# Performance work log

Measured on AMD Instinct MI355X. Metric: run time of the kernel, lower is better.

The kernel has to match this reference:

```python
import jax, jax.numpy as jnp
import numpy as np

BN_EPS = 1e-5


def _fps(xyz, n_centers):
    """Furthest point sampling. xyz: (B,N,3) -> idx (B,n_centers) int32.
    Deterministic start at index 0 (torch version uses randint start)."""
    B, N, _ = xyz.shape
    batch_ar = jnp.arange(B)

    def step(carry, _):
        distances, farthest = carry  # (B,N), (B,)
        center = xyz[batch_ar, farthest]  # (B,3)
        d = jnp.sum((xyz - center[:, None, :]) ** 2, axis=-1)  # (B,N)
        distances = jnp.minimum(distances, d)
        new_far = jnp.argmax(distances, axis=-1)
        return (distances, new_far), farthest

    init = (jnp.full((B, N), jnp.inf, dtype=xyz.dtype),
            jnp.zeros((B,), dtype=jnp.int32))
    _, idxs = jax.lax.scan(step, init, None, length=n_centers)  # (n_centers, B)
    return idxs.T  # (B, n_centers)


def _knn_group(xyz, centers, k):
    """xyz:(B,N,3), centers:(B,M,3) -> patches (B,M,k,3) center-relative."""
    # (B,M,N) squared distances
    dists = jnp.sum((centers[:, :, None, :] - xyz[:, None, :, :]) ** 2, axis=-1)
    _, idx = jax.lax.top_k(-dists, k)  # (B,M,k) smallest distances
    # gather neighbor coords: (B,M,k,3)
    patches = jnp.take_along_axis(xyz[:, None, :, :], idx[..., None], axis=2)
    return patches - centers[:, :, None, :]


def _bn_eval(x, gamma, beta):
    # BatchNorm1d in eval mode: running_mean=0, running_var=1
    return x * (gamma / jnp.sqrt(1.0 + BN_EPS)) + beta


def _mini_pointnet(patches, W1, b1, g1, bt1, W2, b2, g2, bt2, W3, b3, g3, bt3):
    B, M, k, C = patches.shape
    x = patches.reshape(B * M * k, C)
    x = jax.nn.relu(_bn_eval(x @ W1 + b1, g1, bt1))
    x = jax.nn.relu(_bn_eval(x @ W2 + b2, g2, bt2))
    x = jax.nn.relu(_bn_eval(x @ W3 + b3, g3, bt3))
    x = x.reshape(B * M, k, -1).max(axis=1)
    return x.reshape(B, M, -1)


def setup_inputs() -> dict:
    key = jax.random.key(0)
    ks = jax.random.split(key, 8)
    B, N = 16, 16384
    embed = 256

    def lin(kk, fan_in, fan_out):
        bound = 1.0 / np.sqrt(fan_in)
        k1, k2 = jax.random.split(kk)
        W = jax.random.uniform(k1, (fan_in, fan_out), jnp.float32, -bound, bound)
        b = jax.random.uniform(k2, (fan_out,), jnp.float32, -bound, bound)
        return W, b

    W1, b1 = lin(ks[1], 3, 64)
    W2, b2 = lin(ks[2], 64, 128)
    W3, b3 = lin(ks[3], 128, embed)
    return {
        "xyz": jax.random.normal(ks[0], (B, N, 3), jnp.float32),
        "W1": W1, "b1": b1, "g1": jnp.ones((64,)), "bt1": jnp.zeros((64,)),
        "W2": W2, "b2": b2, "g2": jnp.ones((128,)), "bt2": jnp.zeros((128,)),
        "W3": W3, "b3": b3, "g3": jnp.ones((embed,)), "bt3": jnp.zeros((embed,)),
        "n_centers": 256,
        "k": 32,
    }


def reference(xyz, W1, b1, g1, bt1, W2, b2, g2, bt2, W3, b3, g3, bt3,
              n_centers, k):
    center_idx = _fps(xyz, n_centers)  # (B, M)
    centers = jnp.take_along_axis(xyz, center_idx[..., None], axis=1)  # (B,M,3)
    patches = _knn_group(xyz, centers, k)  # (B,M,k,3)
    tokens = _mini_pointnet(patches, W1, b1, g1, bt1, W2, b2, g2, bt2,
                            W3, b3, g3, bt3)
    return tokens, centers
```

## Files before the change

kernel.cpp:

```cpp
#include <hip/hip_runtime.h>

constexpr int B   = 16;
constexpr int N   = 16384;
constexpr int M   = 256;
constexpr int K   = 32;
constexpr int EMB = 256;

__device__ __forceinline__ float sqdist(float px, float py, float pz,
                                        float cx, float cy, float cz) {
  float dx = __fsub_rn(px, cx);
  float dy = __fsub_rn(py, cy);
  float dz = __fsub_rn(pz, cz);
  return __fadd_rn(__fadd_rn(__fmul_rn(dx, dx), __fmul_rn(dy, dy)),
                   __fmul_rn(dz, dz));
}

constexpr int FT = 1024;
constexpr int FW = FT / 64;

#define FPS_REP16(X) X(0) X(1) X(2) X(3) X(4) X(5) X(6) X(7) X(8) X(9) \
  X(10) X(11) X(12) X(13) X(14) X(15)

__global__ __launch_bounds__(FT) void fps_kernel(
    const float* __restrict__ xyz, float* __restrict__ centers) {
  const int b = blockIdx.x;
  const int tid = threadIdx.x;
  const float* base = xyz + (size_t)b * N * 3;
  const float4* b4 = (const float4*)base;

#define FPS_DECL(i) float ds##i = __builtin_inff();
  FPS_REP16(FPS_DECL)
#undef FPS_DECL

  __shared__ float s_pv[2][FW];
  __shared__ int s_pn[2][FW];

  float cx = base[0], cy = base[1], cz = base[2];

  const int f0 = tid * 12;

  for (int it = 0; it < M; ++it) {
    if (tid == 0) {
      float* co = centers + ((size_t)b * M + it) * 3;
      co[0] = cx; co[1] = cy; co[2] = cz;
    }
    const int p = it & 1;

    float bv = -1.0f;
    int bj = 0;

#define FPS_UPD(dn, j, X, Y, Z) {                          \
    float dx = __fsub_rn((X), cx);                         \
    float dy = __fsub_rn((Y), cy);                         \
    float dz = __fsub_rn((Z), cz);                         \
    float dd = __fadd_rn(__fadd_rn(__fmul_rn(dx, dx),      \
                                   __fmul_rn(dy, dy)),     \
                         __fmul_rn(dz, dz));               \
    float nd = fminf(dn, dd);                              \
    dn = nd;                                               \
    bool g = nd > bv;                                      \
    bv = g ? nd : bv;                                      \
    bj = g ? (j) : bj; }

#define FPS_CHUNK(c, dA, dB, dC, dD) {                     \
    float4 qa = b4[f0 + (c) * 3 + 0];                      \
    float4 qb = b4[f0 + (c) * 3 + 1];                      \
    float4 qc = b4[f0 + (c) * 3 + 2];                      \
    FPS_UPD(dA, (c) * 4 + 0, qa.x, qa.y, qa.z)             \
    FPS_UPD(dB, (c) * 4 + 1, qa.w, qb.x, qb.y)             \
    FPS_UPD(dC, (c) * 4 + 2, qb.z, qb.w, qc.x)             \
    FPS_UPD(dD, (c) * 4 + 3, qc.y, qc.z, qc.w) }

    FPS_CHUNK(0, ds0, ds1, ds2, ds3)
    FPS_CHUNK(1, ds4, ds5, ds6, ds7)
    FPS_CHUNK(2, ds8, ds9, ds10, ds11)
    FPS_CHUNK(3, ds12, ds13, ds14, ds15)
#undef FPS_CHUNK
#undef FPS_UPD

    int bn = (tid << 4) + bj;

#pragma unroll
    for (int mm = 32; mm >= 1; mm >>= 1) {
      float ov = __shfl_xor(bv, mm, 64);
      int on = __shfl_xor(bn, mm, 64);
      if (ov > bv || (ov == bv && on < bn)) { bv = ov; bn = on; }
    }
    if ((tid & 63) == 0) { s_pv[p][tid >> 6] = bv; s_pn[p][tid >> 6] = bn; }
    __syncthreads();

    float v = s_pv[p][0];
    int n = s_pn[p][0];
#pragma unroll
    for (int w = 1; w < FW; ++w) {
      float ov = s_pv[p][w];
      int on = s_pn[p][w];
      if (ov > v || (ov == v && on < n)) { v = ov; n = on; }
    }
    cx = base[(size_t)n * 3 + 0];
    cy = base[(size_t)n * 3 + 1];
    cz = base[(size_t)n * 3 + 2];
  }
}

constexpr int KT = 256;
constexpr int CAP = 512;
constexpr int NBUCKET = 1024;

__global__ __launch_bounds__(KT) void knn_kernel(
    const float* __restrict__ xyz, const float* __restrict__ centers,
    float* __restrict__ patches) {
  const int blk = blockIdx.x;
  const int b = blk >> 8;
  const int tid = threadIdx.x;
  const float* base = xyz + (size_t)b * N * 3;

  __shared__ int hist[NBUCKET];
  __shared__ unsigned cb[CAP];
  __shared__ int ci[CAP];
  __shared__ int s_nin, s_ncand, s_tb;
  __shared__ int s_wsum[KT / 64];
  __shared__ float s_cc[3];

  if (tid == 0) {
    const float* c = centers + (size_t)blk * 3;
    s_cc[0] = c[0]; s_cc[1] = c[1]; s_cc[2] = c[2];
    s_nin = 0; s_ncand = 0;
  }
  for (int i = tid; i < NBUCKET; i += KT) hist[i] = 0;
  __syncthreads();

  const float cx = s_cc[0], cy = s_cc[1], cz = s_cc[2];

  for (int n = tid; n < N; n += KT) {
    float d = sqdist(base[n * 3], base[n * 3 + 1], base[n * 3 + 2], cx, cy, cz);
    atomicAdd(&hist[__float_as_uint(d) >> 21], 1);
  }
  __syncthreads();

  int h0[4];
  int loc = 0;
#pragma unroll
  for (int i = 0; i < 4; ++i) { h0[i] = hist[tid * 4 + i]; loc += h0[i]; }
  int lane = tid & 63, wid = tid >> 6;
  int scan = loc;
  for (int off = 1; off < 64; off <<= 1) {
    int o = __shfl_up(scan, off, 64);
    if (lane >= off) scan += o;
  }
  if (lane == 63) s_wsum[wid] = scan;
  __syncthreads();
  int woff = 0;
  for (int w = 0; w < wid; ++w) woff += s_wsum[w];
  int c0 = woff + scan - loc;
#pragma unroll
  for (int i = 0; i < 4; ++i) {
    int c1 = c0 + h0[i];
    if (c0 < K && c1 >= K) s_tb = tid * 4 + i;
    c0 = c1;
  }
  __syncthreads();
  const int tb = s_tb;
  const unsigned lo = (unsigned)tb << 21;
  const unsigned hi = (unsigned)(tb + 1) << 21;

  for (int n = tid; n < N; n += KT) {
    float x = base[n * 3], y = base[n * 3 + 1], z = base[n * 3 + 2];
    float d = sqdist(x, y, z, cx, cy, cz);
    unsigned bits = __float_as_uint(d);
    if (bits < lo) {
      int pos = atomicAdd(&s_nin, 1);
      float* p = patches + ((size_t)blk * K + pos) * 3;
      p[0] = __fsub_rn(x, cx); p[1] = __fsub_rn(y, cy); p[2] = __fsub_rn(z, cz);
    } else if (bits < hi) {
      int q = atomicAdd(&s_ncand, 1);
      if (q < CAP) { cb[q] = bits; ci[q] = n; }
    }
  }
  __syncthreads();

  const int nin = s_nin;
  const int ncand = min(s_ncand, CAP);
  const int nsel = K - nin;
  for (int j = tid; j < ncand; j += KT) {
    unsigned bj = cb[j];
    int ij = ci[j];
    int rank = 0;
    for (int i2 = 0; i2 < ncand; ++i2) {
      unsigned bv = cb[i2];
      int iv = ci[i2];
      rank += (bv < bj || (bv == bj && iv < ij)) ? 1 : 0;
    }
    if (rank < nsel) {
      float x = base[ij * 3], y = base[ij * 3 + 1], z = base[ij * 3 + 2];
      float* p = patches + ((size_t)blk * K + nin + rank) * 3;
      p[0] = __fsub_rn(x, cx); p[1] = __fsub_rn(y, cy); p[2] = __fsub_rn(z, cz);
    }
  }
}

constexpr int MT = 128;

__global__ __launch_bounds__(MT) void mlp_kernel(
    const float* __restrict__ patches,
    const float* __restrict__ W1, const float* __restrict__ b1,
    const float* __restrict__ g1, const float* __restrict__ bt1,
    const float* __restrict__ W2, const float* __restrict__ b2,
    const float* __restrict__ g2, const float* __restrict__ bt2,
    const float* __restrict__ W3, const float* __restrict__ b3,
    const float* __restrict__ g3, const float* __restrict__ bt3,
    float* __restrict__ tokens) {
  const int pm = blockIdx.x;
  const int tid = threadIdx.x;
  __shared__ float xs[3][K];
  __shared__ float h1s[64 * K];
  __shared__ float h2s[128 * K];
  __shared__ float pms[2][EMB];

  const float* patch = patches + (size_t)pm * (K * 3);
  if (tid < 96) xs[tid % 3][tid / 3] = patch[tid];
  __syncthreads();

  const int cg = tid & 63;
  const int half = tid >> 6;
  const int pt0 = half * 16;
  const float rs = 1.0f / sqrtf(1.0f + 1e-5f);

  {
    const int c = cg;
    const float w0 = W1[c], w1 = W1[64 + c], w2 = W1[128 + c];
    const float bb = b1[c];
    const float sc = g1[c] * rs, be = bt1[c];
    float o[16];
#pragma unroll
    for (int p = 0; p < 16; ++p) {
      int pt = pt0 + p;
      float a = xs[0][pt] * w0 + xs[1][pt] * w1 + xs[2][pt] * w2 + bb;
      o[p] = fmaxf(a * sc + be, 0.0f);
    }
    const int so = (c & 7) << 2;
#pragma unroll
    for (int p4 = 0; p4 < 16; p4 += 4) {
      *(float4*)&h1s[c * K + ((pt0 + p4) ^ so)] =
          make_float4(o[p4], o[p4 + 1], o[p4 + 2], o[p4 + 3]);
    }
  }
  __syncthreads();

  {
    const int c = cg * 2;
    float acc0[16], acc1[16];
    const float bb0 = b2[c], bb1 = b2[c + 1];
#pragma unroll
    for (int p = 0; p < 16; ++p) { acc0[p] = bb0; acc1[p] = bb1; }
    for (int k = 0; k < 64; ++k) {
      const float2 w = *(const float2*)(W2 + k * 128 + c);
      const int so = (k & 7) << 2;
      float4 x0 = *(const float4*)&h1s[k * K + ((pt0 + 0) ^ so)];
      float4 x1 = *(const float4*)&h1s[k * K + ((pt0 + 4) ^ so)];
      float4 x2 = *(const float4*)&h1s[k * K + ((pt0 + 8) ^ so)];
      float4 x3 = *(const float4*)&h1s[k * K + ((pt0 + 12) ^ so)];
      float xv[16] = {x0.x, x0.y, x0.z, x0.w, x1.x, x1.y, x1.z, x1.w,
                      x2.x, x2.y, x2.z, x2.w, x3.x, x3.y, x3.z, x3.w};
#pragma unroll
      for (int p = 0; p < 16; ++p) {
        acc0[p] += xv[p] * w.x;
        acc1[p] += xv[p] * w.y;
      }
    }
    const float sc0 = g2[c] * rs, be0 = bt2[c];
    const float sc1 = g2[c + 1] * rs, be1 = bt2[c + 1];
    float o0[16], o1[16];
#pragma unroll
    for (int p = 0; p < 16; ++p) {
      o0[p] = fmaxf(acc0[p] * sc0 + be0, 0.0f);
      o1[p] = fmaxf(acc1[p] * sc1 + be1, 0.0f);
    }
    const int soa = (c & 7) << 2, sob = ((c + 1) & 7) << 2;
#pragma unroll
    for (int p4 = 0; p4 < 16; p4 += 4) {
      *(float4*)&h2s[c * K + ((pt0 + p4) ^ soa)] =
          make_float4(o0[p4], o0[p4 + 1], o0[p4 + 2], o0[p4 + 3]);
      *(float4*)&h2s[(c + 1) * K + ((pt0 + p4) ^ sob)] =
          make_float4(o1[p4], o1[p4 + 1], o1[p4 + 2], o1[p4 + 3]);
    }
  }
  __syncthreads();

  {
    const int c = cg * 4;
    float acc[4][16];
#pragma unroll
    for (int i = 0; i < 4; ++i) {
      const float bb = b3[c + i];
#pragma unroll
      for (int p = 0; p < 16; ++p) acc[i][p] = bb;
    }
    for (int k = 0; k < 128; ++k) {
      const float4 w = *(const float4*)(W3 + (size_t)k * 256 + c);
      const int so = (k & 7) << 2;
      float4 x0 = *(const float4*)&h2s[k * K + ((pt0 + 0) ^ so)];
      float4 x1 = *(const float4*)&h2s[k * K + ((pt0 + 4) ^ so)];
      float4 x2 = *(const float4*)&h2s[k * K + ((pt0 + 8) ^ so)];
      float4 x3 = *(const float4*)&h2s[k * K + ((pt0 + 12) ^ so)];
      float xv[16] = {x0.x, x0.y, x0.z, x0.w, x1.x, x1.y, x1.z, x1.w,
                      x2.x, x2.y, x2.z, x2.w, x3.x, x3.y, x3.z, x3.w};
#pragma unroll
      for (int p = 0; p < 16; ++p) {
        acc[0][p] += xv[p] * w.x;
        acc[1][p] += xv[p] * w.y;
        acc[2][p] += xv[p] * w.z;
        acc[3][p] += xv[p] * w.w;
      }
    }
#pragma unroll
    for (int i = 0; i < 4; ++i) {
      const float sc = g3[c + i] * rs, be = bt3[c + i];
      float mx = 0.0f;
#pragma unroll
      for (int p = 0; p < 16; ++p)
        mx = fmaxf(mx, fmaxf(acc[i][p] * sc + be, 0.0f));
      pms[half][c + i] = mx;
    }
  }
  __syncthreads();

  {
    const int c2 = tid * 2;
    float* to = tokens + (size_t)pm * EMB;
    to[c2] = fmaxf(pms[0][c2], pms[1][c2]);
    to[c2 + 1] = fmaxf(pms[0][c2 + 1], pms[1][c2 + 1]);
  }
}

extern "C" void kernel_launch(void* const* d_in, const int* in_sizes, int n_in,
                              void* d_out, int out_size, void* d_ws,
                              size_t ws_size, hipStream_t stream) {
  const float* xyz = (const float*)d_in[0];
  const float* W1 = (const float*)d_in[1];
  const float* b1 = (const float*)d_in[2];
  const float* g1 = (const float*)d_in[3];
  const float* bt1 = (const float*)d_in[4];
  const float* W2 = (const float*)d_in[5];
  const float* b2 = (const float*)d_in[6];
  const float* g2 = (const float*)d_in[7];
  const float* bt2 = (const float*)d_in[8];
  const float* W3 = (const float*)d_in[9];
  const float* b3 = (const float*)d_in[10];
  const float* g3 = (const float*)d_in[11];
  const float* bt3 = (const float*)d_in[12];

  float* tokens = (float*)d_out;
  float* centers = tokens + (size_t)B * M * EMB;
  float* patches = (float*)d_ws;

  fps_kernel<<<B, FT, 0, stream>>>(xyz, centers);
  knn_kernel<<<B * M, KT, 0, stream>>>(xyz, centers, patches);
  mlp_kernel<<<B * M, MT, 0, stream>>>(patches, W1, b1, g1, bt1, W2, b2, g2,
                                       bt2, W3, b3, g3, bt3, tokens);
}
```

Before: 947.3 us.

## Stage half of FPS point coordinates and most distances in LDS

```diff
diff --git a/kernel.cpp b/kernel.cpp
--- a/kernel.cpp
+++ b/kernel.cpp
@@ -18,9 +18,6 @@
 constexpr int FT = 1024;
 constexpr int FW = FT / 64;
 
-#define FPS_REP16(X) X(0) X(1) X(2) X(3) X(4) X(5) X(6) X(7) X(8) X(9) \
-  X(10) X(11) X(12) X(13) X(14) X(15)
-
 __global__ __launch_bounds__(FT) void fps_kernel(
     const float* __restrict__ xyz, float* __restrict__ centers) {
   const int b = blockIdx.x;
@@ -28,16 +25,21 @@
   const float* base = xyz + (size_t)b * N * 3;
   const float4* b4 = (const float4*)base;
 
-#define FPS_DECL(i) float ds##i = __builtin_inff();
-  FPS_REP16(FPS_DECL)
-#undef FPS_DECL
-
+  __shared__ float4 s_co[6 * FT];
+  __shared__ float4 s_dA[3 * FT];
   __shared__ float s_pv[2][FW];
   __shared__ int s_pn[2][FW];
 
+  const int f0 = tid * 12;
+#pragma unroll
+  for (int c = 0; c < 6; ++c) s_co[c * FT + tid] = b4[f0 + c];
+  const float inf = __builtin_inff();
+#pragma unroll
+  for (int c = 0; c < 3; ++c) s_dA[c * FT + tid] = make_float4(inf, inf, inf, inf);
+  float ds12 = inf, ds13 = inf, ds14 = inf, ds15 = inf;
+
   float cx = base[0], cy = base[1], cz = base[2];
-
-  const int f0 = tid * 12;
+  __syncthreads();
 
   for (int it = 0; it < M; ++it) {
     if (tid == 0) {
@@ -49,33 +51,51 @@
     float bv = -1.0f;
     int bj = 0;
 
-#define FPS_UPD(dn, j, X, Y, Z) {                          \
+#define FPS_UPD(D, J, X, Y, Z) {                           \
     float dx = __fsub_rn((X), cx);                         \
     float dy = __fsub_rn((Y), cy);                         \
     float dz = __fsub_rn((Z), cz);                         \
     float dd = __fadd_rn(__fadd_rn(__fmul_rn(dx, dx),      \
                                    __fmul_rn(dy, dy)),     \
                          __fmul_rn(dz, dz));               \
-    float nd = fminf(dn, dd);                              \
-    dn = nd;                                               \
+    float nd = fminf(D, dd);                               \
+    D = nd;                                                \
     bool g = nd > bv;                                      \
     bv = g ? nd : bv;                                      \
-    bj = g ? (j) : bj; }
-
-#define FPS_CHUNK(c, dA, dB, dC, dD) {                     \
-    float4 qa = b4[f0 + (c) * 3 + 0];                      \
-    float4 qb = b4[f0 + (c) * 3 + 1];                      \
-    float4 qc = b4[f0 + (c) * 3 + 2];                      \
-    FPS_UPD(dA, (c) * 4 + 0, qa.x, qa.y, qa.z)             \
-    FPS_UPD(dB, (c) * 4 + 1, qa.w, qb.x, qb.y)             \
-    FPS_UPD(dC, (c) * 4 + 2, qb.z, qb.w, qc.x)             \
-    FPS_UPD(dD, (c) * 4 + 3, qc.y, qc.z, qc.w) }
-
-    FPS_CHUNK(0, ds0, ds1, ds2, ds3)
-    FPS_CHUNK(1, ds4, ds5, ds6, ds7)
-    FPS_CHUNK(2, ds8, ds9, ds10, ds11)
-    FPS_CHUNK(3, ds12, ds13, ds14, ds15)
-#undef FPS_CHUNK
+    bj = g ? (J) : bj; }
+
+#define FPS_G4(qa, qb, qc, D0, D1, D2, D3, JB)             \
+    FPS_UPD(D0, (JB) + 0, qa.x, qa.y, qa.z)                \
+    FPS_UPD(D1, (JB) + 1, qa.w, qb.x, qb.y)                \
+    FPS_UPD(D2, (JB) + 2, qb.z, qb.w, qc.x)                \
+    FPS_UPD(D3, (JB) + 3, qc.y, qc.z, qc.w)
+
+    float4 g0 = b4[f0 + 6], g1 = b4[f0 + 7], g2 = b4[f0 + 8];
+
+    {
+      float4 qa = s_co[0 * FT + tid];
+      float4 qb = s_co[1 * FT + tid];
+      float4 qc = s_co[2 * FT + tid];
+      float4 dq = s_dA[0 * FT + tid];
+      FPS_G4(qa, qb, qc, dq.x, dq.y, dq.z, dq.w, 0)
+      s_dA[0 * FT + tid] = dq;
+    }
+    float4 g3 = b4[f0 + 9], g4 = b4[f0 + 10], g5 = b4[f0 + 11];
+    {
+      float4 qa = s_co[3 * FT + tid];
+      float4 qb = s_co[4 * FT + tid];
+      float4 qc = s_co[5 * FT + tid];
+      float4 dq = s_dA[1 * FT + tid];
+      FPS_G4(qa, qb, qc, dq.x, dq.y, dq.z, dq.w, 4)
+      s_dA[1 * FT + tid] = dq;
+    }
+    {
+      float4 dq = s_dA[2 * FT + tid];
+      FPS_G4(g0, g1, g2, dq.x, dq.y, dq.z, dq.w, 8)
+      s_dA[2 * FT + tid] = dq;
+    }
+    FPS_G4(g3, g4, g5, ds12, ds13, ds14, ds15, 12)
+#undef FPS_G4
 #undef FPS_UPD
 
     int bn = (tid << 4) + bj;
```

After: 993.6 us. 1.05x slower.
